# Kernel optimization log

Measured on AMD Instinct MI355X. Metric: run time of the kernel, lower is better.

## Reference

```python
import jax, jax.numpy as jnp
import numpy as np

B, C, D, H, W = 4, 256, 32, 32, 32
K = 1024  # codebook size


def setup_inputs() -> dict:
    key = jax.random.key(0)
    k1, k2 = jax.random.split(key)
    z = jax.random.normal(k1, (B, C, D, H, W), dtype=jnp.float32)
    # torch init: uniform(-1/K, 1/K)
    emb_weight = jax.random.uniform(k2, (K, C), dtype=jnp.float32,
                                    minval=-1.0 / K, maxval=1.0 / K)
    return {"z": z, "emb_weight": emb_weight}


def reference(z, emb_weight):
    beta = 0.25
    emb_dim = emb_weight.shape[1]
    # [B, C, D, H, W] -> [B, D, H, W, C]
    zc = jnp.transpose(z, (0, 2, 3, 4, 1))
    z_flat = zc.reshape(-1, emb_dim)  # [N, C]
    # squared euclidean distances [N, K]
    d = (jnp.sum(z_flat ** 2, axis=1, keepdims=True)
         + jnp.sum(emb_weight ** 2, axis=1)
         - 2.0 * jnp.matmul(z_flat, emb_weight.T))
    idx = jnp.argmin(d, axis=1)  # [N]
    z_q = emb_weight[idx].reshape(zc.shape)  # [B, D, H, W, C]
    sg = jax.lax.stop_gradient
    loss = jnp.mean((sg(z_q) - zc) ** 2) + beta * jnp.mean((z_q - sg(zc)) ** 2)
    # straight-through estimator
    z_q = zc + sg(z_q - zc)
    # back to [B, C, D, H, W]
    z_q = jnp.transpose(z_q, (0, 4, 1, 2, 3))
    return z_q, loss, idx
```

## Files before the change

### kernel.cpp

```cpp
#include <hip/hip_runtime.h>

#define SPATIAL 32768
#define BATCH   4
#define CH      256
#define KCODES  1024
#define NPTS    (BATCH*SPATIAL)
#define ZQ_SIZE (BATCH*CH*SPATIAL)

#define WS_LOSS  0
#define WS_CNT   8
#define WS_ENORM 16
#define WS_EH    4112
#define WS_EL    (WS_EH + KCODES*CH*2)
#define WS_FLAGS (WS_EL + KCODES*CH*2)

#define MARG 1e-4f

typedef _Float16 f16x8 __attribute__((ext_vector_type(8)));
typedef float    f32x4 __attribute__((ext_vector_type(4)));
typedef int      i32x4 __attribute__((ext_vector_type(4)));

__global__ __launch_bounds__(256) void vq_prep(const float* __restrict__ emb,
                                               _Float16* __restrict__ eh,
                                               _Float16* __restrict__ el) {
  int i = blockIdx.x * 256 + threadIdx.x;
  float es = emb[i] * 1024.0f;
  _Float16 h = (_Float16)es;
  eh[i] = h;
  el[i] = (_Float16)(es - (float)h);
}

__global__ __launch_bounds__(256) void vq_enorm(const float* __restrict__ emb,
                                                float* __restrict__ enorm) {
  int k = blockIdx.x * 256 + threadIdx.x;
  const float* e = emb + (size_t)k * CH;
  double s = 0.0;
#pragma unroll 8
  for (int c = 0; c < CH; ++c) s = fma((double)e[c], (double)e[c], s);
  enorm[k] = (float)s;
}

__global__ __launch_bounds__(256) void vq_main(
    const float* __restrict__ z, const _Float16* __restrict__ eh_g,
    const _Float16* __restrict__ el_g, const float* __restrict__ enorm,
    float* __restrict__ out_idx, double* __restrict__ loss_acc,
    int* __restrict__ flag_cnt, int* __restrict__ flags) {
  __shared__ _Float16 zh[64][258];
  __shared__ _Float16 zl[64][258];
  __shared__ float en_s[KCODES];
  __shared__ float znb[64];
  __shared__ float rm1[4][64];
  __shared__ float rm2[4][64];
  __shared__ int   ri1[4][64];

  int tid = threadIdx.x;
  int w = tid >> 6;
  int lane = tid & 63;
  int n0 = blockIdx.x * 64;
  int b = n0 / SPATIAL, s0 = n0 % SPATIAL;
  const float* zb = z + (size_t)b * CH * SPATIAL + s0;

  {
    int pt = tid & 63, crow = tid >> 6;
#pragma unroll 4
    for (int j = 0; j < 64; ++j) {
      int c = crow + 4 * j;
      float v = zb[(size_t)c * SPATIAL + pt];
      _Float16 h = (_Float16)v;
      zh[pt][c] = h;
      zl[pt][c] = (_Float16)(v - (float)h);
    }
  }
#pragma unroll
  for (int j = 0; j < 4; ++j) en_s[tid + 256 * j] = enorm[tid + 256 * j];
  rm1[tid >> 6][tid & 63] = 1e30f;
  rm2[tid >> 6][tid & 63] = 1e30f;
  ri1[tid >> 6][tid & 63] = 0;
  if (tid < 64) {
    double s = 0.0;
    for (int c = 0; c < CH; ++c) {
      float v = zb[(size_t)c * SPATIAL + tid];
      s = fma((double)v, (double)v, s);
    }
    znb[tid] = (float)s;
  }
  __syncthreads();

  int hq = lane >> 4;
  int lr = lane & 15;

  for (int kt = 0; kt < 8; ++kt) {
    int k0 = kt * 128;
    f32x4 acc[4][2];
#pragma unroll
    for (int m = 0; m < 4; ++m)
#pragma unroll
      for (int n = 0; n < 2; ++n) acc[m][n] = (f32x4){0.f, 0.f, 0.f, 0.f};

#pragma unroll 2
    for (int cc = 0; cc < 8; ++cc) {
      int ca = cc * 32 + hq * 8;
      f16x8 ah[4], al[4], bh[2], bl[2];
#pragma unroll
      for (int m = 0; m < 4; ++m) {
        const int* ph = (const int*)&zh[m * 16 + lr][ca];
        const int* pl = (const int*)&zl[m * 16 + lr][ca];
        i32x4 th = {ph[0], ph[1], ph[2], ph[3]};
        i32x4 tl = {pl[0], pl[1], pl[2], pl[3]};
        ah[m] = __builtin_bit_cast(f16x8, th);
        al[m] = __builtin_bit_cast(f16x8, tl);
      }
#pragma unroll
      for (int n = 0; n < 2; ++n) {
        int code = k0 + w * 32 + n * 16 + lr;
        bh[n] = *(const f16x8*)&eh_g[(size_t)code * CH + ca];
        bl[n] = *(const f16x8*)&el_g[(size_t)code * CH + ca];
      }
#pragma unroll
      for (int m = 0; m < 4; ++m)
#pragma unroll
        for (int n = 0; n < 2; ++n) {
          acc[m][n] = __builtin_amdgcn_mfma_f32_16x16x32_f16(ah[m], bh[n], acc[m][n], 0, 0, 0);
          acc[m][n] = __builtin_amdgcn_mfma_f32_16x16x32_f16(al[m], bh[n], acc[m][n], 0, 0, 0);
          acc[m][n] = __builtin_amdgcn_mfma_f32_16x16x32_f16(ah[m], bl[n], acc[m][n], 0, 0, 0);
        }
    }

#pragma unroll
    for (int m = 0; m < 4; ++m) {
#pragma unroll
      for (int r = 0; r < 4; ++r) {
        int pt = m * 16 + hq * 4 + r;
        float zn = znb[pt];
        int c0i = k0 + w * 32 + lr;
        float t0 = zn + en_s[c0i];
        float p0 = t0 - acc[m][0][r] * 0.001953125f;
        float t1 = zn + en_s[c0i + 16];
        float p1 = t1 - acc[m][1][r] * 0.001953125f;
        float m1, m2; int i1;
        if (p1 < p0) { m1 = p1; i1 = c0i + 16; m2 = p0; }
        else         { m1 = p0; i1 = c0i;      m2 = p1; }
#pragma unroll
        for (int msk = 1; msk <= 8; msk <<= 1) {
          float om1 = __shfl_xor(m1, msk);
          float om2 = __shfl_xor(m2, msk);
          int   oi1 = __shfl_xor(i1, msk);
          if (om1 < m1 || (om1 == m1 && oi1 < i1)) {
            m2 = fminf(m1, om2); m1 = om1; i1 = oi1;
          } else {
            m2 = fminf(m2, om1);
          }
        }
        if (lr == 0) {
          float cm1 = rm1[w][pt];
          if (m1 < cm1 || (m1 == cm1 && i1 < ri1[w][pt])) {
            rm2[w][pt] = fminf(cm1, m2);
            rm1[w][pt] = m1; ri1[w][pt] = i1;
          } else {
            rm2[w][pt] = fminf(rm2[w][pt], m1);
          }
        }
      }
    }
  }
  __syncthreads();

  double dv = 0.0;
  if (tid < 64) {
    float m1 = rm1[0][tid], m2 = rm2[0][tid];
    int i1 = ri1[0][tid];
#pragma unroll
    for (int pq = 1; pq < 4; ++pq) {
      float a1 = rm1[pq][tid], a2 = rm2[pq][tid];
      int ai = ri1[pq][tid];
      if (a1 < m1 || (a1 == m1 && ai < i1)) {
        m2 = fminf(m1, a2); m1 = a1; i1 = ai;
      } else {
        m2 = fminf(m2, a1);
      }
    }
    int n = n0 + tid;
    out_idx[n] = (float)i1;
    if (m2 - m1 <= MARG) {
      int p = atomicAdd(flag_cnt, 1);
      if (p < NPTS) flags[p] = n;
    }
    dv = (double)m1;
  }
  if (tid < 64) {
#pragma unroll
    for (int msk = 1; msk < 64; msk <<= 1) dv += __shfl_xor(dv, msk);
    if (tid == 0) atomicAdd(loss_acc, dv);
  }
}

__global__ __launch_bounds__(256) void vq_recheck(
    const float* __restrict__ z, const float* __restrict__ emb,
    const float* __restrict__ enorm, const int* __restrict__ flag_cnt,
    const int* __restrict__ flags, float* __restrict__ out_idx) {
  __shared__ float zs[4][CH];
  __shared__ float znf[4];
  __shared__ float bm[256];
  __shared__ int   bi[256];
  int cnt = *flag_cnt; if (cnt > NPTS) cnt = NPTS;
  int t = threadIdx.x;
  for (int base = blockIdx.x * 4; base < cnt; base += gridDim.x * 4) {
#pragma unroll
    for (int q = 0; q < 4; ++q) {
      int ii = base + q; if (ii >= cnt) ii = cnt - 1;
      int n = flags[ii];
      int b = n / SPATIAL, s = n % SPATIAL;
      zs[q][t] = z[((size_t)b * CH + t) * SPATIAL + s];
    }
    __syncthreads();
    if (t < 4) {
      double sd = 0.0;
      for (int c = 0; c < CH; ++c) sd = fma((double)zs[t][c], (double)zs[t][c], sd);
      znf[t] = (float)sd;
    }
    __syncthreads();
    float best[4] = {1e30f, 1e30f, 1e30f, 1e30f};
    int besti[4] = {0, 0, 0, 0};
    for (int q = 0; q < 4; ++q) {
      int code = t + 256 * q;
      const float* er = emb + (size_t)code * CH;
      float g0 = 0.f, g1 = 0.f, g2 = 0.f, g3 = 0.f;
#pragma unroll 8
      for (int c = 0; c < CH; ++c) {
        float e = er[c];
        g0 = fmaf(zs[0][c], e, g0);
        g1 = fmaf(zs[1][c], e, g1);
        g2 = fmaf(zs[2][c], e, g2);
        g3 = fmaf(zs[3][c], e, g3);
      }
      float en = enorm[code];
      float d0 = (znf[0] + en) - 2.f * g0;
      float d1 = (znf[1] + en) - 2.f * g1;
      float d2 = (znf[2] + en) - 2.f * g2;
      float d3 = (znf[3] + en) - 2.f * g3;
      if (d0 < best[0]) { best[0] = d0; besti[0] = code; }
      if (d1 < best[1]) { best[1] = d1; besti[1] = code; }
      if (d2 < best[2]) { best[2] = d2; besti[2] = code; }
      if (d3 < best[3]) { best[3] = d3; besti[3] = code; }
    }
#pragma unroll
    for (int p = 0; p < 4; ++p) {
      bm[t] = best[p]; bi[t] = besti[p];
      __syncthreads();
      for (int off = 128; off > 0; off >>= 1) {
        if (t < off) {
          float ob = bm[t + off]; int oi = bi[t + off];
          if (ob < bm[t] || (ob == bm[t] && oi < bi[t])) { bm[t] = ob; bi[t] = oi; }
        }
        __syncthreads();
      }
      int ii = base + p;
      if (t == 0 && ii < cnt) out_idx[flags[ii]] = (float)bi[0];
      __syncthreads();
    }
  }
}

__global__ __launch_bounds__(256) void vq_scatter(
    const float* __restrict__ emb, const float* __restrict__ out_idx,
    float* __restrict__ zq, const double* __restrict__ loss_acc,
    float* __restrict__ loss_out) {
  int c = blockIdx.y, b = blockIdx.z;
  int s = (blockIdx.x * 256 + threadIdx.x) * 4;
  int nb = b * SPATIAL + s;
  int i0 = (int)out_idx[nb + 0];
  int i1 = (int)out_idx[nb + 1];
  int i2 = (int)out_idx[nb + 2];
  int i3 = (int)out_idx[nb + 3];
  float4 o;
  o.x = emb[(size_t)i0 * CH + c];
  o.y = emb[(size_t)i1 * CH + c];
  o.z = emb[(size_t)i2 * CH + c];
  o.w = emb[(size_t)i3 * CH + c];
  *reinterpret_cast<float4*>(&zq[((size_t)(b * CH + c)) * SPATIAL + s]) = o;
  if (blockIdx.x == 0 && blockIdx.y == 0 && blockIdx.z == 0 && threadIdx.x == 0)
    loss_out[0] = (float)(loss_acc[0] * 1.25 / (double)ZQ_SIZE);
}

extern "C" void kernel_launch(void* const* d_in, const int* in_sizes, int n_in,
                              void* d_out, int out_size, void* d_ws, size_t ws_size,
                              hipStream_t stream) {
  const float* z   = (const float*)d_in[0];
  const float* emb = (const float*)d_in[1];
  float* out = (float*)d_out;
  char* ws = (char*)d_ws;

  double*   loss_acc = (double*)(ws + WS_LOSS);
  int*      flag_cnt = (int*)(ws + WS_CNT);
  float*    enorm    = (float*)(ws + WS_ENORM);
  _Float16* eh       = (_Float16*)(ws + WS_EH);
  _Float16* el       = (_Float16*)(ws + WS_EL);
  int*      flags    = (int*)(ws + WS_FLAGS);

  float* loss_out = out + ZQ_SIZE;
  float* out_idx  = out + ZQ_SIZE + 1;

  hipMemsetAsync(d_ws, 0, 16, stream);
  vq_prep<<<KCODES * CH / 256, 256, 0, stream>>>(emb, eh, el);
  vq_enorm<<<KCODES / 256, 256, 0, stream>>>(emb, enorm);
  vq_main<<<NPTS / 64, 256, 0, stream>>>(z, eh, el, enorm, out_idx,
                                         loss_acc, flag_cnt, flags);
  vq_recheck<<<512, 256, 0, stream>>>(z, emb, enorm, flag_cnt, flags, out_idx);
  vq_scatter<<<dim3(SPATIAL / 1024, CH, BATCH), 256, 0, stream>>>(
      emb, out_idx, out, loss_acc, loss_out);
}
```

Measured before the change: 773.0 us.

## Keep per-lane running argmin in registers and defer shuffle reduction

Each lane now keeps its running top-2 minimum and index in registers across all code tiles, with the cross-lane shuffle reduction done once at the end instead of once per tile. Code norms and point norms are held in registers rather than shared memory. The z staging now uses vectorized 16-byte LDS stores with padding changed to 264, and the z-norm is computed in the same pass as the load instead of a separate serial loop in 64 threads. The near-tie margin is widened, which may flag more points for the fp32 recheck, and the extra per-lane state raises register pressure.

```diff
diff --git a/kernel.cpp b/kernel.cpp
--- a/kernel.cpp
+++ b/kernel.cpp
@@ -14,11 +14,10 @@
 #define WS_EL    (WS_EH + KCODES*CH*2)
 #define WS_FLAGS (WS_EL + KCODES*CH*2)
 
-#define MARG 1e-4f
+#define MARG 1.5e-4f
 
 typedef _Float16 f16x8 __attribute__((ext_vector_type(8)));
 typedef float    f32x4 __attribute__((ext_vector_type(4)));
-typedef int      i32x4 __attribute__((ext_vector_type(4)));
 
 __global__ __launch_bounds__(256) void vq_prep(const float* __restrict__ emb,
                                                _Float16* __restrict__ eh,
@@ -45,13 +44,13 @@
     const _Float16* __restrict__ el_g, const float* __restrict__ enorm,
     float* __restrict__ out_idx, double* __restrict__ loss_acc,
     int* __restrict__ flag_cnt, int* __restrict__ flags) {
-  __shared__ _Float16 zh[64][258];
-  __shared__ _Float16 zl[64][258];
-  __shared__ float en_s[KCODES];
-  __shared__ float znb[64];
-  __shared__ float rm1[4][64];
-  __shared__ float rm2[4][64];
-  __shared__ int   ri1[4][64];
+  __shared__ _Float16 zh[64][264];
+  __shared__ _Float16 zl[64][264];
+  __shared__ double   znp[4][64];
+  __shared__ float    znb[64];
+  __shared__ float rm1s[4][64];
+  __shared__ float rm2s[4][64];
+  __shared__ int   ri1s[4][64];
 
   int tid = threadIdx.x;
   int w = tid >> 6;
@@ -61,33 +60,51 @@
   const float* zb = z + (size_t)b * CH * SPATIAL + s0;
 
   {
-    int pt = tid & 63, crow = tid >> 6;
-#pragma unroll 4
-    for (int j = 0; j < 64; ++j) {
-      int c = crow + 4 * j;
-      float v = zb[(size_t)c * SPATIAL + pt];
-      _Float16 h = (_Float16)v;
-      zh[pt][c] = h;
-      zl[pt][c] = (_Float16)(v - (float)h);
-    }
-  }
-#pragma unroll
-  for (int j = 0; j < 4; ++j) en_s[tid + 256 * j] = enorm[tid + 256 * j];
-  rm1[tid >> 6][tid & 63] = 1e30f;
-  rm2[tid >> 6][tid & 63] = 1e30f;
-  ri1[tid >> 6][tid & 63] = 0;
-  if (tid < 64) {
-    double s = 0.0;
-    for (int c = 0; c < CH; ++c) {
-      float v = zb[(size_t)c * SPATIAL + tid];
-      s = fma((double)v, (double)v, s);
-    }
-    znb[tid] = (float)s;
-  }
+    int pt = lane, crow = w;
+    const float* zcol = zb + pt;
+    double zacc = 0.0;
+#pragma unroll
+    for (int oct = 0; oct < 8; ++oct) {
+      int c0 = crow * 64 + oct * 8;
+      f16x8 h8, l8;
+#pragma unroll
+      for (int i = 0; i < 8; ++i) {
+        float v = zcol[(size_t)(c0 + i) * SPATIAL];
+        zacc = fma((double)v, (double)v, zacc);
+        _Float16 h = (_Float16)v;
+        h8[i] = h;
+        l8[i] = (_Float16)(v - (float)h);
+      }
+      *(f16x8*)&zh[pt][c0] = h8;
+      *(f16x8*)&zl[pt][c0] = l8;
+    }
+    znp[crow][pt] = zacc;
+  }
+  __syncthreads();
+  if (tid < 64)
+    znb[tid] = (float)(znp[0][tid] + znp[1][tid] + znp[2][tid] + znp[3][tid]);
   __syncthreads();
 
   int hq = lane >> 4;
   int lr = lane & 15;
+
+  float en_reg[16];
+#pragma unroll
+  for (int kt = 0; kt < 8; ++kt) {
+    en_reg[kt * 2]     = enorm[kt * 128 + w * 32 + lr];
+    en_reg[kt * 2 + 1] = enorm[kt * 128 + w * 32 + lr + 16];
+  }
+  float znr[16];
+#pragma unroll
+  for (int m = 0; m < 4; ++m)
+#pragma unroll
+    for (int r = 0; r < 4; ++r)
+      znr[m * 4 + r] = znb[m * 16 + hq * 4 + r];
+
+  float rm1[16], rm2[16];
+  int   ri1[16];
+#pragma unroll
+  for (int q = 0; q < 16; ++q) { rm1[q] = 1e30f; rm2[q] = 1e30f; ri1[q] = 0; }
 
   for (int kt = 0; kt < 8; ++kt) {
     int k0 = kt * 128;
@@ -103,12 +120,8 @@
       f16x8 ah[4], al[4], bh[2], bl[2];
 #pragma unroll
       for (int m = 0; m < 4; ++m) {
-        const int* ph = (const int*)&zh[m * 16 + lr][ca];
-        const int* pl = (const int*)&zl[m * 16 + lr][ca];
-        i32x4 th = {ph[0], ph[1], ph[2], ph[3]};
-        i32x4 tl = {pl[0], pl[1], pl[2], pl[3]};
-        ah[m] = __builtin_bit_cast(f16x8, th);
-        al[m] = __builtin_bit_cast(f16x8, tl);
+        ah[m] = *(const f16x8*)&zh[m * 16 + lr][ca];
+        al[m] = *(const f16x8*)&zl[m * 16 + lr][ca];
       }
 #pragma unroll
       for (int n = 0; n < 2; ++n) {
@@ -126,40 +139,45 @@
         }
     }
 
+    float enA = en_reg[kt * 2], enB = en_reg[kt * 2 + 1];
+    int c0i = k0 + w * 32 + lr;
 #pragma unroll
     for (int m = 0; m < 4; ++m) {
 #pragma unroll
       for (int r = 0; r < 4; ++r) {
+        int q = m * 4 + r;
+        float zn = znr[q];
+        float p0 = (zn + enA) - acc[m][0][r] * 0x1p-9f;
+        float p1 = (zn + enB) - acc[m][1][r] * 0x1p-9f;
+        if (p0 < rm1[q]) { rm2[q] = rm1[q]; rm1[q] = p0; ri1[q] = c0i; }
+        else             { rm2[q] = fminf(rm2[q], p0); }
+        if (p1 < rm1[q]) { rm2[q] = rm1[q]; rm1[q] = p1; ri1[q] = c0i + 16; }
+        else             { rm2[q] = fminf(rm2[q], p1); }
+      }
+    }
+  }
+
+#pragma unroll
+  for (int m = 0; m < 4; ++m) {
+#pragma unroll
+    for (int r = 0; r < 4; ++r) {
+      int q = m * 4 + r;
+      float m1 = rm1[q], m2 = rm2[q];
+      int i1 = ri1[q];
+#pragma unroll
+      for (int msk = 1; msk <= 8; msk <<= 1) {
+        float om1 = __shfl_xor(m1, msk);
+        float om2 = __shfl_xor(m2, msk);
+        int   oi1 = __shfl_xor(i1, msk);
+        if (om1 < m1 || (om1 == m1 && oi1 < i1)) {
+          m2 = fminf(m1, om2); m1 = om1; i1 = oi1;
+        } else {
+          m2 = fminf(m2, om1);
+        }
+      }
+      if (lr == 0) {
         int pt = m * 16 + hq * 4 + r;
-        float zn = znb[pt];
-        int c0i = k0 + w * 32 + lr;
-        float t0 = zn + en_s[c0i];
-        float p0 = t0 - acc[m][0][r] * 0.001953125f;
-        float t1 = zn + en_s[c0i + 16];
-        float p1 = t1 - acc[m][1][r] * 0.001953125f;
-        float m1, m2; int i1;
-        if (p1 < p0) { m1 = p1; i1 = c0i + 16; m2 = p0; }
-        else         { m1 = p0; i1 = c0i;      m2 = p1; }
-#pragma unroll
-        for (int msk = 1; msk <= 8; msk <<= 1) {
-          float om1 = __shfl_xor(m1, msk);
-          float om2 = __shfl_xor(m2, msk);
-          int   oi1 = __shfl_xor(i1, msk);
-          if (om1 < m1 || (om1 == m1 && oi1 < i1)) {
-            m2 = fminf(m1, om2); m1 = om1; i1 = oi1;
-          } else {
-            m2 = fminf(m2, om1);
-          }
-        }
-        if (lr == 0) {
-          float cm1 = rm1[w][pt];
-          if (m1 < cm1 || (m1 == cm1 && i1 < ri1[w][pt])) {
-            rm2[w][pt] = fminf(cm1, m2);
-            rm1[w][pt] = m1; ri1[w][pt] = i1;
-          } else {
-            rm2[w][pt] = fminf(rm2[w][pt], m1);
-          }
-        }
+        rm1s[w][pt] = m1; rm2s[w][pt] = m2; ri1s[w][pt] = i1;
       }
     }
   }
@@ -167,12 +185,12 @@
 
   double dv = 0.0;
   if (tid < 64) {
-    float m1 = rm1[0][tid], m2 = rm2[0][tid];
-    int i1 = ri1[0][tid];
+    float m1 = rm1s[0][tid], m2 = rm2s[0][tid];
+    int i1 = ri1s[0][tid];
 #pragma unroll
     for (int pq = 1; pq < 4; ++pq) {
-      float a1 = rm1[pq][tid], a2 = rm2[pq][tid];
-      int ai = ri1[pq][tid];
+      float a1 = rm1s[pq][tid], a2 = rm2s[pq][tid];
+      int ai = ri1s[pq][tid];
       if (a1 < m1 || (a1 == m1 && ai < i1)) {
         m2 = fminf(m1, a2); m1 = a1; i1 = ai;
       } else {
@@ -186,8 +204,6 @@
       if (p < NPTS) flags[p] = n;
     }
     dv = (double)m1;
-  }
-  if (tid < 64) {
 #pragma unroll
     for (int msk = 1; msk < 64; msk <<= 1) dv += __shfl_xor(dv, msk);
     if (tid == 0) atomicAdd(loss_acc, dv);
```

New measurement: 623.9 us. -19.3%, faster.
